# Kernel tuning notes

Measured on AMD Instinct MI355X. Metric: run time of the kernel, lower is better.

The kernel has to match this reference:

```python
import jax, jax.numpy as jnp
import numpy as np
import math

WS = (8, 8)        # window_size for context (2D)
HEADS = 8


def _attend(q, k, v, h):
    # q: (Bw, Nq, inner), k/v: (Bw, Nk, inner)
    Bw, Nq, inner = q.shape
    d = inner // h
    q = q.reshape(Bw, Nq, h, d)
    k = k.reshape(Bw, -1, h, d)
    v = v.reshape(Bw, -1, h, d)
    scores = jnp.einsum('bqhd,bkhd->bhqk', q, k) * (d ** -0.5)
    attn = jax.nn.softmax(scores, axis=-1)
    out = jnp.einsum('bhqk,bkhd->bqhd', attn, v)
    return out.reshape(Bw, Nq, inner)


def reference(x, context, W_q, W_k, W_v, W_out, b_out):
    B, C, T, H, W = x.shape
    H_, W_ = context.shape[-2], context.shape[-1]
    ws = WS
    assert H_ * W_ > ws[0] * ws[1] and H * W >= ws[0] * ws[1]  # window branch
    # pad context to multiple of window_size (no-op for chosen shapes)
    pad_r_2d = (-W_) % ws[1]
    pad_b_2d = (-H_) % ws[0]
    context = jnp.pad(context, ((0, 0), (0, 0), (0, pad_b_2d), (0, pad_r_2d)))
    # scaled window size for the (smaller) 3D query tensor
    ws_ = (math.ceil(float(ws[0]) * H / H_), math.ceil(float(ws[1]) * W / W_))
    pad_r_3d = (-W) % ws_[1]
    pad_b_3d = (-H) % ws_[0]
    x = jnp.pad(x, ((0, 0), (0, 0), (0, 0), (0, pad_b_3d), (0, pad_r_3d)))
    Hp, Wp = x.shape[-2], x.shape[-1]
    Hc, Wc = context.shape[-2], context.shape[-1]
    # window partition: context (B,C,Hc,Wc) -> (B*h*w, ws0*ws1, C)
    hc, wc = Hc // ws[0], Wc // ws[1]
    ctx = context.reshape(B, C, hc, ws[0], wc, ws[1])
    ctx = ctx.transpose(0, 2, 4, 3, 5, 1).reshape(B * hc * wc, ws[0] * ws[1], C)
    # window partition: x (B,C,T,Hp,Wp) -> (B*h*w, T*ws_0*ws_1, C)
    hg, wg = Hp // ws_[0], Wp // ws_[1]
    xw = x.reshape(B, C, T, hg, ws_[0], wg, ws_[1])
    xw = xw.transpose(0, 3, 5, 2, 4, 6, 1).reshape(B * hg * wg, T * ws_[0] * ws_[1], C)
    # QKV projections (no bias: qkv_bias=False, to_k always bias-free)
    q = xw @ W_q
    k = ctx @ W_k
    v = ctx @ W_v
    out = _attend(q, k, v, HEADS)  # (Bw, Nq, inner)
    inner = out.shape[-1]
    # window reverse -> (B, inner, T, Hp, Wp)
    out = out.reshape(B, hg, wg, T, ws_[0], ws_[1], inner)
    out = out.transpose(0, 6, 3, 1, 4, 2, 5).reshape(B, inner, T, Hp, Wp)
    out = out[:, :, :, :H, :W]
    # b c t h w -> b (t h w) c
    out = out.transpose(0, 2, 3, 4, 1).reshape(B, T * H * W, inner)
    return out @ W_out + b_out


def setup_inputs() -> dict:
    key = jax.random.key(0)
    ks = jax.random.split(key, 7)
    D = 512
    s = 0.02
    return {
        'x': jax.random.normal(ks[0], (4, D, 4, 32, 32), jnp.float32),
        'context': jax.random.normal(ks[1], (4, D, 128, 128), jnp.float32),
        'W_q': jax.random.normal(ks[2], (D, D), jnp.float32) * s,
        'W_k': jax.random.normal(ks[3], (D, D), jnp.float32) * s,
        'W_v': jax.random.normal(ks[4], (D, D), jnp.float32) * s,
        'W_out': jax.random.normal(ks[5], (D, D), jnp.float32) * s,
        'b_out': jnp.zeros((D,), jnp.float32),
    }
```

## Files before the change

kernel.cpp:

```cpp
#include <hip/hip_runtime.h>
#include <hip/hip_bf16.h>

typedef unsigned short u16;
typedef unsigned int u32;
typedef __attribute__((ext_vector_type(4))) float f32x4;
typedef __attribute__((ext_vector_type(4))) u16 u16x4;
typedef __attribute__((ext_vector_type(8))) u16 u16x8;
typedef __attribute__((ext_vector_type(8))) short s16x8;

__device__ __forceinline__ u16 f2bf(float f) {
    union { float f; u32 u; } v; v.f = f;
    u32 r = v.u + 0x7FFFu + ((v.u >> 16) & 1u);
    return (u16)(r >> 16);
}

__device__ __forceinline__ void gl_lds16(const u16* g, u16* l) {
    __builtin_amdgcn_global_load_lds(
        (const __attribute__((address_space(1))) unsigned int*)(const void*)g,
        (__attribute__((address_space(3))) unsigned int*)(void*)l, 16, 0, 0);
}

__global__ __launch_bounds__(256) void wtrans_kernel(
    const float* __restrict__ w0, const float* __restrict__ w1,
    const float* __restrict__ w2, const float* __restrict__ w3,
    u16* __restrict__ dst) {
    __shared__ float t[64][65];
    int wsel = blockIdx.x >> 6;
    int tile = blockIdx.x & 63;
    int j0 = (tile >> 3) * 64, c0 = (tile & 7) * 64;
    const float* src = wsel == 0 ? w0 : wsel == 1 ? w1 : wsel == 2 ? w2 : w3;
    u16* out = dst + (long)wsel * 512 * 512;
    int tj = threadIdx.x & 63;
    int ti = threadIdx.x >> 6;
#pragma unroll
    for (int p = 0; p < 16; ++p) {
        int row = p * 4 + ti;
        t[row][tj] = src[(long)(c0 + row) * 512 + j0 + tj];
    }
    __syncthreads();
#pragma unroll
    for (int p = 0; p < 16; ++p) {
        int jl = p * 4 + ti;
        out[(long)(j0 + jl) * 512 + c0 + tj] = f2bf(t[tj][jl]);
    }
}

__global__ __launch_bounds__(256) void permx_kernel(const float* __restrict__ x, u16* __restrict__ Aq) {
    __shared__ u16 t[64][36];
    int bid = blockIdx.x;
    int cb = bid & 7; bid >>= 3;
    int y  = bid & 31; bid >>= 5;
    int tt = bid & 3; bid >>= 2;
    int b  = bid;
    int tid = threadIdx.x;
    long ibase = ((long)(b * 512 + cb * 64) * 4 + tt) * 1024 + y * 32;
#pragma unroll
    for (int p = 0; p < 2; ++p) {
        int task = p * 256 + tid;
        int cc = task >> 3, xl = (task & 7) * 4;
        float4 v = *(const float4*)&x[ibase + (long)cc * 4096 + xl];
        u16x4 o = {f2bf(v.x), f2bf(v.y), f2bf(v.z), f2bf(v.w)};
        *(u16x4*)&t[cc][xl] = o;
    }
    __syncthreads();
    {
        int xx = tid >> 3, j = tid & 7;
        u16x8 o;
#pragma unroll
        for (int i = 0; i < 8; ++i) o[i] = t[j * 8 + i][xx];
        int row = b * 4096 + (y >> 1) * 256 + (xx >> 1) * 16 + tt * 4 + (y & 1) * 2 + (xx & 1);
        *(u16x8*)&Aq[(long)row * 512 + cb * 64 + j * 8] = o;
    }
}

__global__ __launch_bounds__(256) void permc_kernel(const float* __restrict__ ctx, u16* __restrict__ Actx) {
    __shared__ u16 t[64][68];
    int bid = blockIdx.x;
    int cb = bid & 7; bid >>= 3;
    int xb = bid & 1; bid >>= 1;
    int y  = bid & 127; bid >>= 7;
    int b  = bid;
    int tid = threadIdx.x;
    long ibase = ((long)(b * 512 + cb * 64) * 128 + y) * 128 + xb * 64;
#pragma unroll
    for (int p = 0; p < 4; ++p) {
        int task = p * 256 + tid;
        int cc = task >> 4, xl = (task & 15) * 4;
        float4 v = *(const float4*)&ctx[ibase + (long)cc * 16384 + xl];
        u16x4 o = {f2bf(v.x), f2bf(v.y), f2bf(v.z), f2bf(v.w)};
        *(u16x4*)&t[cc][xl] = o;
    }
    __syncthreads();
#pragma unroll
    for (int p = 0; p < 2; ++p) {
        int task = p * 256 + tid;
        int xx = task >> 3, j = task & 7;
        u16x8 o;
#pragma unroll
        for (int i = 0; i < 8; ++i) o[i] = t[j * 8 + i][xx];
        int xg = xb * 64 + xx;
        int row = b * 16384 + (y >> 3) * 1024 + (xg >> 3) * 64 + (y & 7) * 8 + (xg & 7);
        *(u16x8*)&Actx[(long)row * 512 + cb * 64 + j * 8] = o;
    }
}

template <int FINAL>
__global__ __launch_bounds__(256, 4) void gemm128_kernel(
    const u16* __restrict__ A, const u16* __restrict__ Bt,
    u16* __restrict__ Cb, float* __restrict__ Cf, const float* __restrict__ bias) {
    __shared__ u16 As[1024 * 8];
    __shared__ u16 Bs[1024 * 8];
    int tid = threadIdx.x;
    int lane = tid & 63;
    int w = tid >> 6;
    int wm = w >> 1, wn = w & 1;
    int bid = blockIdx.x;
    int wg = (bid & 7) * 64 + (bid >> 3);
    int m0 = (wg >> 2) * 128;
    int n0 = (wg & 3) * 128;

    const f32x4 z = {0.f, 0.f, 0.f, 0.f};
    f32x4 acc[4][4];
#pragma unroll
    for (int i = 0; i < 4; ++i)
#pragma unroll
        for (int j = 0; j < 4; ++j) acc[i][j] = z;

    int aoff[4], boff[4], lb[4];
#pragma unroll
    for (int i = 0; i < 4; ++i) {
        int s = i * 256 + tid;
        int row = s >> 3;
        int cb = (s & 7) ^ (row & 7);
        aoff[i] = (m0 + row) * 512 + cb * 8;
        boff[i] = (n0 + row) * 512 + cb * 8;
        lb[i] = (i * 256 + w * 64) * 8;
    }
    int la = lane & 15, lg = lane >> 4;
    for (int ks = 0; ks < 8; ++ks) {
        int ko = ks * 64;
#pragma unroll
        for (int i = 0; i < 4; ++i) {
            gl_lds16(&A[aoff[i] + ko], &As[lb[i]]);
            gl_lds16(&Bt[boff[i] + ko], &Bs[lb[i]]);
        }
        __syncthreads();
#pragma unroll
        for (int kk = 0; kk < 2; ++kk) {
            int cb = kk * 4 + lg;
            s16x8 af[4], bfr[4];
#pragma unroll
            for (int mt = 0; mt < 4; ++mt) {
                int r = wm * 64 + mt * 16 + la;
                af[mt] = *(const s16x8*)&As[r * 64 + ((cb ^ (r & 7)) * 8)];
            }
#pragma unroll
            for (int nt = 0; nt < 4; ++nt) {
                int c = wn * 64 + nt * 16 + la;
                bfr[nt] = *(const s16x8*)&Bs[c * 64 + ((cb ^ (c & 7)) * 8)];
            }
#pragma unroll
            for (int mt = 0; mt < 4; ++mt)
#pragma unroll
                for (int nt = 0; nt < 4; ++nt)
                    acc[mt][nt] = __builtin_amdgcn_mfma_f32_16x16x32_bf16(af[mt], bfr[nt], acc[mt][nt], 0, 0, 0);
        }
        __syncthreads();
    }
#pragma unroll
    for (int mt = 0; mt < 4; ++mt) {
#pragma unroll
        for (int nt = 0; nt < 4; ++nt) {
            int col = n0 + wn * 64 + nt * 16 + la;
#pragma unroll
            for (int rr = 0; rr < 4; ++rr) {
                int r = m0 + wm * 64 + mt * 16 + lg * 4 + rr;
                float v = acc[mt][nt][rr];
                if (FINAL) {
                    int bb = r >> 12, hg = (r >> 8) & 15, wgx = (r >> 4) & 15;
                    int tt = (r >> 2) & 3, rr0 = (r >> 1) & 1, cc0 = r & 1;
                    int tok = bb * 4096 + tt * 1024 + (hg * 2 + rr0) * 32 + wgx * 2 + cc0;
                    Cf[(long)tok * 512 + col] = v + bias[col];
                } else {
                    Cb[(long)r * 512 + col] = f2bf(v);
                }
            }
        }
    }
}

__global__ __launch_bounds__(256, 4) void gemmkv_kernel(
    const u16* __restrict__ A, const u16* __restrict__ Bk, const u16* __restrict__ Bv,
    u16* __restrict__ CK, u16* __restrict__ CV) {
    __shared__ u16 As[1024 * 8];
    __shared__ u16 Bks[512 * 8];
    __shared__ u16 Bvs[512 * 8];
    int tid = threadIdx.x;
    int lane = tid & 63;
    int w = tid >> 6;
    int kv = w >> 1, wr = w & 1;
    int bid = blockIdx.x;
    int wg = (bid & 7) * 512 + (bid >> 3);
    int m0 = (wg >> 3) * 128;
    int n0 = (wg & 7) * 64;

    const f32x4 z = {0.f, 0.f, 0.f, 0.f};
    f32x4 acc[4][4];
#pragma unroll
    for (int i = 0; i < 4; ++i)
#pragma unroll
        for (int j = 0; j < 4; ++j) acc[i][j] = z;

    int aoff[4], lba[4];
#pragma unroll
    for (int i = 0; i < 4; ++i) {
        int s = i * 256 + tid;
        int row = s >> 3;
        int cb = (s & 7) ^ (row & 7);
        aoff[i] = (m0 + row) * 512 + cb * 8;
        lba[i] = (i * 256 + w * 64) * 8;
    }
    int boff[2], lbb[2];
#pragma unroll
    for (int i = 0; i < 2; ++i) {
        int s = i * 256 + tid;
        int row = s >> 3;
        int cb = (s & 7) ^ (row & 7);
        boff[i] = (n0 + row) * 512 + cb * 8;
        lbb[i] = (i * 256 + w * 64) * 8;
    }
    int la = lane & 15, lg = lane >> 4;
    for (int ks = 0; ks < 8; ++ks) {
        int ko = ks * 64;
#pragma unroll
        for (int i = 0; i < 4; ++i) gl_lds16(&A[aoff[i] + ko], &As[lba[i]]);
#pragma unroll
        for (int i = 0; i < 2; ++i) {
            gl_lds16(&Bk[boff[i] + ko], &Bks[lbb[i]]);
            gl_lds16(&Bv[boff[i] + ko], &Bvs[lbb[i]]);
        }
        __syncthreads();
        const u16* Bsel = kv ? Bvs : Bks;
#pragma unroll
        for (int kk = 0; kk < 2; ++kk) {
            int cb = kk * 4 + lg;
            s16x8 af[4], bfr[4];
#pragma unroll
            for (int mt = 0; mt < 4; ++mt) {
                int r = wr * 64 + mt * 16 + la;
                af[mt] = *(const s16x8*)&As[r * 64 + ((cb ^ (r & 7)) * 8)];
            }
#pragma unroll
            for (int nt = 0; nt < 4; ++nt) {
                int c = nt * 16 + la;
                bfr[nt] = *(const s16x8*)&Bsel[c * 64 + ((cb ^ (c & 7)) * 8)];
            }
#pragma unroll
            for (int mt = 0; mt < 4; ++mt)
#pragma unroll
                for (int nt = 0; nt < 4; ++nt)
                    acc[mt][nt] = __builtin_amdgcn_mfma_f32_16x16x32_bf16(af[mt], bfr[nt], acc[mt][nt], 0, 0, 0);
        }
        __syncthreads();
    }
    u16* C = kv ? CV : CK;
#pragma unroll
    for (int mt = 0; mt < 4; ++mt) {
#pragma unroll
        for (int nt = 0; nt < 4; ++nt) {
            int col = n0 + nt * 16 + la;
#pragma unroll
            for (int rr = 0; rr < 4; ++rr) {
                int r = m0 + wr * 64 + mt * 16 + lg * 4 + rr;
                C[(long)r * 512 + col] = f2bf(acc[mt][nt][rr]);
            }
        }
    }
}

__global__ __launch_bounds__(64) void attn_kernel(
    const u16* __restrict__ Q, const u16* __restrict__ K,
    const u16* __restrict__ V, u16* __restrict__ O) {
    __shared__ u16 P[16 * 104];
    int bid = blockIdx.x;
    int wg = (bid & 7) * 1024 + (bid >> 3);
    int win = wg >> 3;
    int h = wg & 7;
    int lane = threadIdx.x;
    int la = lane & 15, lg = lane >> 4;
    const u16* Qb = Q + (long)win * 16 * 512 + h * 64;
    const u16* Kb = K + (long)win * 64 * 512 + h * 64;
    const u16* Vb = V + (long)win * 64 * 512 + h * 64;

    s16x8 qf[2];
#pragma unroll
    for (int kk = 0; kk < 2; ++kk)
        qf[kk] = *(const s16x8*)&Qb[la * 512 + kk * 32 + lg * 8];

    const f32x4 z = {0.f, 0.f, 0.f, 0.f};
    f32x4 st[4];
#pragma unroll
    for (int rt = 0; rt < 4; ++rt) st[rt] = z;
#pragma unroll
    for (int rt = 0; rt < 4; ++rt)
#pragma unroll
        for (int kk = 0; kk < 2; ++kk) {
            s16x8 kf = *(const s16x8*)&Kb[(rt * 16 + la) * 512 + kk * 32 + lg * 8];
            st[rt] = __builtin_amdgcn_mfma_f32_16x16x32_bf16(kf, qf[kk], st[rt], 0, 0, 0);
        }
    float mloc = -1e30f;
#pragma unroll
    for (int rt = 0; rt < 4; ++rt)
#pragma unroll
        for (int rr = 0; rr < 4; ++rr) {
            st[rt][rr] *= 0.125f;
            mloc = fmaxf(mloc, st[rt][rr]);
        }
    mloc = fmaxf(mloc, __shfl_xor(mloc, 16));
    mloc = fmaxf(mloc, __shfl_xor(mloc, 32));
    float p[4][4];
    float sloc = 0.f;
#pragma unroll
    for (int rt = 0; rt < 4; ++rt)
#pragma unroll
        for (int rr = 0; rr < 4; ++rr) {
            p[rt][rr] = __expf(st[rt][rr] - mloc);
            sloc += p[rt][rr];
        }
    sloc += __shfl_xor(sloc, 16);
    sloc += __shfl_xor(sloc, 32);
    float inv = 1.0f / sloc;
#pragma unroll
    for (int rt = 0; rt < 4; ++rt)
#pragma unroll
        for (int rr = 0; rr < 4; ++rr)
            P[la * 104 + rt * 16 + lg * 4 + rr] = f2bf(p[rt][rr] * inv);
    __syncthreads();

    f32x4 od[4];
#pragma unroll
    for (int dt = 0; dt < 4; ++dt) od[dt] = z;
#pragma unroll
    for (int kk2 = 0; kk2 < 2; ++kk2) {
        s16x8 pa = *(const s16x8*)&P[la * 104 + kk2 * 32 + lg * 8];
#pragma unroll
        for (int dt = 0; dt < 4; ++dt) {
            s16x8 vb;
#pragma unroll
            for (int j = 0; j < 8; ++j)
                vb[j] = (short)Vb[(long)(kk2 * 32 + lg * 8 + j) * 512 + dt * 16 + la];
            od[dt] = __builtin_amdgcn_mfma_f32_16x16x32_bf16(pa, vb, od[dt], 0, 0, 0);
        }
    }
    u16* Ob = O + (long)win * 16 * 512 + h * 64;
#pragma unroll
    for (int dt = 0; dt < 4; ++dt)
#pragma unroll
        for (int rr = 0; rr < 4; ++rr)
            Ob[(long)(lg * 4 + rr) * 512 + dt * 16 + la] = f2bf(od[dt][rr]);
}

__global__ void sentinel_kernel(float* out) {
    if (threadIdx.x == 0 && blockIdx.x == 0) out[0] = -12345.0f;
}

extern "C" void kernel_launch(void* const* d_in, const int* in_sizes, int n_in,
                              void* d_out, int out_size, void* d_ws, size_t ws_size,
                              hipStream_t stream) {
    const float* x   = (const float*)d_in[0];
    const float* ctx = (const float*)d_in[1];
    const float* Wq  = (const float*)d_in[2];
    const float* Wk  = (const float*)d_in[3];
    const float* Wv  = (const float*)d_in[4];
    const float* Wo  = (const float*)d_in[5];
    const float* bo  = (const float*)d_in[6];
    float* out = (float*)d_out;

    u16* wsb  = (u16*)d_ws;
    u16* WT   = wsb;
    u16* Aq   = WT + 4l * 262144;
    u16* Actx = Aq + 8388608l;
    u16* Qb   = Actx + 33554432l;
    u16* Kb   = Qb + 8388608l;
    u16* Vb   = Kb + 33554432l;
    u16* Ob   = Vb + 33554432l;
    size_t need = (size_t)(126877696l) * 2;
    if (ws_size < need) {
        sentinel_kernel<<<1, 64, 0, stream>>>(out);
        return;
    }

    wtrans_kernel<<<256, 256, 0, stream>>>(Wq, Wk, Wv, Wo, WT);
    permx_kernel<<<4096, 256, 0, stream>>>(x, Aq);
    permc_kernel<<<8192, 256, 0, stream>>>(ctx, Actx);
    gemm128_kernel<0><<<512, 256, 0, stream>>>(Aq, WT, Qb, nullptr, nullptr);
    gemmkv_kernel<<<4096, 256, 0, stream>>>(Actx, WT + 262144l, WT + 2l * 262144, Kb, Vb);
    attn_kernel<<<8192, 64, 0, stream>>>(Qb, Kb, Vb, Ob);
    gemm128_kernel<1><<<512, 256, 0, stream>>>(Ob, WT + 3l * 262144, nullptr, out, bo);
}
```

Measured before the change: 224.2 us.

## Fuse K/V projections into one 256x256-tile double-buffered GEMM with interleaved output

Replaces the 128x64 K/V GEMM with a single GEMM over a concatenated [Wk;Wv] weight (N=1024), using 256x256 tiles, 512 threads, and double-buffered LDS staging with manual waitcnt/barriers and MFMA priority boosts. K and V are written interleaved into one buffer with row stride 1024, and the attention kernel is updated to read that layout. The aim is to cut redundant A-tile loads and raise arithmetic intensity while overlapping loads with MFMA. In exchange it uses more LDS and registers, which lowers occupancy, and it relies on the transposed K and V weights sitting next to each other in memory.

New measurement: 206.0 us. 8.1% less time.

```diff
diff --git a/kernel.cpp b/kernel.cpp
--- a/kernel.cpp
+++ b/kernel.cpp
@@ -189,98 +189,110 @@
     }
 }
 
-__global__ __launch_bounds__(256, 4) void gemmkv_kernel(
-    const u16* __restrict__ A, const u16* __restrict__ Bk, const u16* __restrict__ Bv,
-    u16* __restrict__ CK, u16* __restrict__ CV) {
-    __shared__ u16 As[1024 * 8];
-    __shared__ u16 Bks[512 * 8];
-    __shared__ u16 Bvs[512 * 8];
+__global__ __launch_bounds__(512, 2) void gemmkv256_kernel(
+    const u16* __restrict__ A, const u16* __restrict__ B, u16* __restrict__ C) {
+    __shared__ u16 lds[2][2][16384];
     int tid = threadIdx.x;
     int lane = tid & 63;
     int w = tid >> 6;
-    int kv = w >> 1, wr = w & 1;
+    int wm = w >> 2, wn = w & 3;
+    int la = lane & 15, lg = lane >> 4;
     int bid = blockIdx.x;
-    int wg = (bid & 7) * 512 + (bid >> 3);
-    int m0 = (wg >> 3) * 128;
-    int n0 = (wg & 7) * 64;
+    int wg = (bid & 7) * 128 + (bid >> 3);
+    int m0 = (wg >> 2) * 256;
+    int n0 = (wg & 3) * 256;
 
     const f32x4 z = {0.f, 0.f, 0.f, 0.f};
-    f32x4 acc[4][4];
-#pragma unroll
-    for (int i = 0; i < 4; ++i)
+    f32x4 acc[8][4];
+#pragma unroll
+    for (int i = 0; i < 8; ++i)
 #pragma unroll
         for (int j = 0; j < 4; ++j) acc[i][j] = z;
 
-    int aoff[4], lba[4];
+    int aoff[4], boff[4], lsl[4];
 #pragma unroll
     for (int i = 0; i < 4; ++i) {
-        int s = i * 256 + tid;
+        int s = i * 512 + tid;
         int row = s >> 3;
         int cb = (s & 7) ^ (row & 7);
         aoff[i] = (m0 + row) * 512 + cb * 8;
-        lba[i] = (i * 256 + w * 64) * 8;
-    }
-    int boff[2], lbb[2];
-#pragma unroll
-    for (int i = 0; i < 2; ++i) {
-        int s = i * 256 + tid;
-        int row = s >> 3;
-        int cb = (s & 7) ^ (row & 7);
         boff[i] = (n0 + row) * 512 + cb * 8;
-        lbb[i] = (i * 256 + w * 64) * 8;
-    }
-    int la = lane & 15, lg = lane >> 4;
-    for (int ks = 0; ks < 8; ++ks) {
-        int ko = ks * 64;
-#pragma unroll
-        for (int i = 0; i < 4; ++i) gl_lds16(&A[aoff[i] + ko], &As[lba[i]]);
-#pragma unroll
-        for (int i = 0; i < 2; ++i) {
-            gl_lds16(&Bk[boff[i] + ko], &Bks[lbb[i]]);
-            gl_lds16(&Bv[boff[i] + ko], &Bvs[lbb[i]]);
-        }
-        __syncthreads();
-        const u16* Bsel = kv ? Bvs : Bks;
+        lsl[i] = (i * 512 + w * 64) * 8;
+    }
+
+    auto STAGE = [&](int t, int buf) {
+#pragma unroll
+        for (int i = 0; i < 4; ++i) {
+            gl_lds16(&A[aoff[i] + t * 64], &lds[buf][0][lsl[i]]);
+            gl_lds16(&B[boff[i] + t * 64], &lds[buf][1][lsl[i]]);
+        }
+    };
+    auto COMPUTE = [&](int buf) {
+        const u16* Ab = lds[buf][0];
+        const u16* Bb = lds[buf][1];
 #pragma unroll
         for (int kk = 0; kk < 2; ++kk) {
             int cb = kk * 4 + lg;
-            s16x8 af[4], bfr[4];
-#pragma unroll
-            for (int mt = 0; mt < 4; ++mt) {
-                int r = wr * 64 + mt * 16 + la;
-                af[mt] = *(const s16x8*)&As[r * 64 + ((cb ^ (r & 7)) * 8)];
+            s16x8 af[8], bfr[4];
+#pragma unroll
+            for (int mt = 0; mt < 8; ++mt) {
+                int r = wm * 128 + mt * 16 + la;
+                af[mt] = *(const s16x8*)&Ab[r * 64 + ((cb ^ (r & 7)) * 8)];
             }
 #pragma unroll
             for (int nt = 0; nt < 4; ++nt) {
-                int c = nt * 16 + la;
-                bfr[nt] = *(const s16x8*)&Bsel[c * 64 + ((cb ^ (c & 7)) * 8)];
-            }
-#pragma unroll
-            for (int mt = 0; mt < 4; ++mt)
+                int c = wn * 64 + nt * 16 + la;
+                bfr[nt] = *(const s16x8*)&Bb[c * 64 + ((cb ^ (c & 7)) * 8)];
+            }
+            __builtin_amdgcn_s_setprio(1);
+#pragma unroll
+            for (int mt = 0; mt < 8; ++mt)
 #pragma unroll
                 for (int nt = 0; nt < 4; ++nt)
                     acc[mt][nt] = __builtin_amdgcn_mfma_f32_16x16x32_bf16(af[mt], bfr[nt], acc[mt][nt], 0, 0, 0);
-        }
-        __syncthreads();
-    }
-    u16* C = kv ? CV : CK;
-#pragma unroll
-    for (int mt = 0; mt < 4; ++mt) {
+            __builtin_amdgcn_s_setprio(0);
+        }
+    };
+
+    STAGE(0, 0);
+    STAGE(1, 1);
+    asm volatile("s_waitcnt vmcnt(8)" ::: "memory");
+    __builtin_amdgcn_s_barrier();
+    asm volatile("" ::: "memory");
+
+#pragma unroll
+    for (int t = 0; t < 8; ++t) {
+        COMPUTE(t & 1);
+        if (t < 6) {
+            asm volatile("" ::: "memory");
+            __builtin_amdgcn_s_barrier();
+            STAGE(t + 2, t & 1);
+            asm volatile("s_waitcnt vmcnt(8)" ::: "memory");
+            __builtin_amdgcn_s_barrier();
+            asm volatile("" ::: "memory");
+        } else if (t == 6) {
+            asm volatile("s_waitcnt vmcnt(0)" ::: "memory");
+            __builtin_amdgcn_s_barrier();
+            asm volatile("" ::: "memory");
+        }
+    }
+
+#pragma unroll
+    for (int mt = 0; mt < 8; ++mt) {
 #pragma unroll
         for (int nt = 0; nt < 4; ++nt) {
-            int col = n0 + nt * 16 + la;
+            int col = n0 + wn * 64 + nt * 16 + la;
 #pragma unroll
             for (int rr = 0; rr < 4; ++rr) {
-                int r = m0 + wr * 64 + mt * 16 + lg * 4 + rr;
-                C[(long)r * 512 + col] = f2bf(acc[mt][nt][rr]);
+                int r = m0 + wm * 128 + mt * 16 + lg * 4 + rr;
+                C[(long)r * 1024 + col] = f2bf(acc[mt][nt][rr]);
             }
         }
     }
 }
 
 __global__ __launch_bounds__(64) void attn_kernel(
-    const u16* __restrict__ Q, const u16* __restrict__ K,
-    const u16* __restrict__ V, u16* __restrict__ O) {
+    const u16* __restrict__ Q, const u16* __restrict__ KV, u16* __restrict__ O) {
     __shared__ u16 P[16 * 104];
     int bid = blockIdx.x;
     int wg = (bid & 7) * 1024 + (bid >> 3);
@@ -289,8 +301,8 @@
     int lane = threadIdx.x;
     int la = lane & 15, lg = lane >> 4;
     const u16* Qb = Q + (long)win * 16 * 512 + h * 64;
-    const u16* Kb = K + (long)win * 64 * 512 + h * 64;
-    const u16* Vb = V + (long)win * 64 * 512 + h * 64;
+    const u16* Kb = KV + (long)win * 64 * 1024 + h * 64;
+    const u16* Vb = KV + (long)win * 64 * 1024 + 512 + h * 64;
 
     s16x8 qf[2];
 #pragma unroll
@@ -305,7 +317,7 @@
     for (int rt = 0; rt < 4; ++rt)
 #pragma unroll
         for (int kk = 0; kk < 2; ++kk) {
-            s16x8 kf = *(const s16x8*)&Kb[(rt * 16 + la) * 512 + kk * 32 + lg * 8];
+            s16x8 kf = *(const s16x8*)&Kb[(rt * 16 + la) * 1024 + kk * 32 + lg * 8];
             st[rt] = __builtin_amdgcn_mfma_f32_16x16x32_bf16(kf, qf[kk], st[rt], 0, 0, 0);
         }
     float mloc = -1e30f;
@@ -348,7 +360,7 @@
             s16x8 vb;
 #pragma unroll
             for (int j = 0; j < 8; ++j)
-                vb[j] = (short)Vb[(long)(kk2 * 32 + lg * 8 + j) * 512 + dt * 16 + la];
+                vb[j] = (short)Vb[(long)(kk2 * 32 + lg * 8 + j) * 1024 + dt * 16 + la];
             od[dt] = __builtin_amdgcn_mfma_f32_16x16x32_bf16(pa, vb, od[dt], 0, 0, 0);
         }
     }
@@ -381,9 +393,8 @@
     u16* Aq   = WT + 4l * 262144;
     u16* Actx = Aq + 8388608l;
     u16* Qb   = Actx + 33554432l;
-    u16* Kb   = Qb + 8388608l;
-    u16* Vb   = Kb + 33554432l;
-    u16* Ob   = Vb + 33554432l;
+    u16* KVb  = Qb + 8388608l;
+    u16* Ob   = KVb + 67108864l;
     size_t need = (size_t)(126877696l) * 2;
     if (ws_size < need) {
         sentinel_kernel<<<1, 64, 0, stream>>>(out);
@@ -394,7 +405,7 @@
     permx_kernel<<<4096, 256, 0, stream>>>(x, Aq);
     permc_kernel<<<8192, 256, 0, stream>>>(ctx, Actx);
     gemm128_kernel<0><<<512, 256, 0, stream>>>(Aq, WT, Qb, nullptr, nullptr);
-    gemmkv_kernel<<<4096, 256, 0, stream>>>(Actx, WT + 262144l, WT + 2l * 262144, Kb, Vb);
-    attn_kernel<<<8192, 64, 0, stream>>>(Qb, Kb, Vb, Ob);
+    gemmkv256_kernel<<<1024, 512, 0, stream>>>(Actx, WT + 262144l, KVb);
+    attn_kernel<<<8192, 64, 0, stream>>>(Qb, KVb, Ob);
     gemm128_kernel<1><<<512, 256, 0, stream>>>(Ob, WT + 3l * 262144, nullptr, out, bo);
 }
```
